# Optimization experiments

Measured on AMD Instinct MI355X. Metric: run time of the kernel, lower is better.

Reference implementation:

```python
import jax, jax.numpy as jnp
import numpy as np

D_MODEL = 1024
N_HEADS = 16
HEAD_DIM = D_MODEL // N_HEADS
D_FF = 4096
ROPE_RANK = 16
LN_EPS = 1e-5


def _ln(x, g, b):
    mu = jnp.mean(x, axis=-1, keepdims=True)
    var = jnp.mean((x - mu) ** 2, axis=-1, keepdims=True)
    return (x - mu) * jax.lax.rsqrt(var + LN_EPS) * g + b


def _rope(x, A, B_):
    # x: [B, T, D]; learned low-rank additive correction to sin/cos tables
    B, T, D = x.shape
    pos = jnp.arange(T, dtype=jnp.float32)
    theta = 1.0 / (10000.0 ** (jnp.arange(0, D, 2, dtype=jnp.float32) / D))  # [D/2]
    angles = pos[:, None] * theta[None, :]                                   # [T, D/2]
    sin_pos, cos_pos = jnp.sin(angles), jnp.cos(angles)
    base = jnp.concatenate([sin_pos, cos_pos], axis=-1)                      # [T, D]
    learned = (base @ A) @ B_                                                # [T, D]
    l_sin, l_cos = jnp.split(learned, 2, axis=-1)
    sin_f = sin_pos + l_sin                                                  # [T, D/2]
    cos_f = cos_pos + l_cos
    xe, xo = x[..., ::2], x[..., 1::2]
    re = xe * cos_f[None] - xo * sin_f[None]
    ro = xe * sin_f[None] + xo * cos_f[None]
    return jnp.stack([re, ro], axis=-1).reshape(B, T, D)


def setup_inputs() -> dict:
    key = jax.random.key(0)
    ks = jax.random.split(key, 20)
    B, T = 2, 2048
    s = 1.0 / np.sqrt(D_MODEL)
    sf = 1.0 / np.sqrt(D_FF)
    sr = 1.0 / np.sqrt(ROPE_RANK)
    return {
        "tgt": jax.random.normal(ks[0], (B, T, D_MODEL), jnp.float32),
        "Wq": jax.random.normal(ks[1], (D_MODEL, D_MODEL), jnp.float32) * s,
        "bq": jnp.zeros((D_MODEL,), jnp.float32),
        "Wk": jax.random.normal(ks[2], (D_MODEL, D_MODEL), jnp.float32) * s,
        "bk": jnp.zeros((D_MODEL,), jnp.float32),
        "Wv": jax.random.normal(ks[3], (D_MODEL, D_MODEL), jnp.float32) * s,
        "bv": jnp.zeros((D_MODEL,), jnp.float32),
        "Wo": jax.random.normal(ks[4], (D_MODEL, D_MODEL), jnp.float32) * s,
        "bo": jnp.zeros((D_MODEL,), jnp.float32),
        "W1": jax.random.normal(ks[5], (D_MODEL, D_FF), jnp.float32) * s,
        "b1": jnp.zeros((D_FF,), jnp.float32),
        "W2": jax.random.normal(ks[6], (D_FF, D_MODEL), jnp.float32) * sf,
        "b2": jnp.zeros((D_MODEL,), jnp.float32),
        "ln1_g": jnp.ones((D_MODEL,), jnp.float32),
        "ln1_b": jnp.zeros((D_MODEL,), jnp.float32),
        "ln2_g": jnp.ones((D_MODEL,), jnp.float32),
        "ln2_b": jnp.zeros((D_MODEL,), jnp.float32),
        "rope_A": jax.random.normal(ks[7], (D_MODEL, ROPE_RANK), jnp.float32) * s,
        "rope_B": jax.random.normal(ks[8], (ROPE_RANK, D_MODEL), jnp.float32) * sr,
    }


def reference(tgt, Wq, bq, Wk, bk, Wv, bv, Wo, bo, W1, b1, W2, b2,
              ln1_g, ln1_b, ln2_g, ln2_b, rope_A, rope_B):
    x = tgt
    B, T, D = x.shape
    q = _rope(x @ Wq + bq, rope_A, rope_B)
    k = _rope(x @ Wk + bk, rope_A, rope_B)
    v = x @ Wv + bv
    # [B, H, T, hd]
    q = q.reshape(B, T, N_HEADS, HEAD_DIM).transpose(0, 2, 1, 3)
    k = k.reshape(B, T, N_HEADS, HEAD_DIM).transpose(0, 2, 1, 3)
    v = v.reshape(B, T, N_HEADS, HEAD_DIM).transpose(0, 2, 1, 3)
    scores = jnp.einsum("bhqd,bhkd->bhqk", q, k) / np.sqrt(HEAD_DIM)
    attn = jax.nn.softmax(scores, axis=-1)  # no mask: module applies none
    ctx = jnp.einsum("bhqk,bhkd->bhqd", attn, v)
    ctx = ctx.transpose(0, 2, 1, 3).reshape(B, T, D)
    x = x + (ctx @ Wo + bo)
    x = _ln(x, ln1_g, ln1_b)
    ff = jax.nn.relu(x @ W1 + b1) @ W2 + b2
    x = _ln(x + ff, ln2_g, ln2_b)
    return x
```

## Files before the change

kernel.cpp:

```cpp
#include <hip/hip_runtime.h>
#include <math.h>

typedef unsigned short u16;
typedef unsigned int u32;
typedef __attribute__((ext_vector_type(8))) short short8v;
typedef __attribute__((ext_vector_type(4))) float f32x4;

__device__ __forceinline__ u16 f2bf(float f) {
    u32 u = __float_as_uint(f);
    u32 r = (u + 0x7fffu + ((u >> 16) & 1u)) >> 16;
    return (u16)r;
}

#define GLOAD_LDS(g, l)                                                        \
    __builtin_amdgcn_global_load_lds(                                          \
        (const __attribute__((address_space(1))) void*)(g),                    \
        (__attribute__((address_space(3))) void*)(l), 16, 0, 0)

#define SCHED_FENCE() __builtin_amdgcn_sched_barrier(0)

__global__ void cast_k(const float* __restrict__ x, u16* __restrict__ y) {
    const int gid = blockIdx.x * blockDim.x + threadIdx.x;
    float4 v = ((const float4*)x)[gid];
    ushort4 o;
    o.x = f2bf(v.x); o.y = f2bf(v.y); o.z = f2bf(v.z); o.w = f2bf(v.w);
    ((ushort4*)y)[gid] = o;
}

__global__ __launch_bounds__(256) void tcast_k(const float* __restrict__ S,
                                               u16* __restrict__ Dt,
                                               int K, int N) {
    __shared__ float tile[32][33];
    const int n0 = blockIdx.x * 32, k0 = blockIdx.y * 32;
    const int tx = threadIdx.x & 31, ty = threadIdx.x >> 5;
#pragma unroll
    for (int i = 0; i < 4; i++)
        tile[ty + 8 * i][tx] = S[(size_t)(k0 + ty + 8 * i) * N + n0 + tx];
    __syncthreads();
#pragma unroll
    for (int i = 0; i < 4; i++)
        Dt[(size_t)(n0 + ty + 8 * i) * K + k0 + tx] = f2bf(tile[tx][ty + 8 * i]);
}

__global__ __launch_bounds__(256) void vtrans_k(const u16* __restrict__ vv,
                                                u16* __restrict__ Vt) {
    __shared__ u16 tile[32][33];
    const int key0 = blockIdx.x * 32, d0 = blockIdx.y * 32, bh = blockIdx.z;
    const int b = bh >> 4, h = bh & 15;
    const int tx = threadIdx.x & 31, ty = threadIdx.x >> 5;
#pragma unroll
    for (int i = 0; i < 4; i++)
        tile[ty + 8 * i][tx] =
            vv[(size_t)(b * 2048 + key0 + ty + 8 * i) * 1024 + h * 64 + d0 + tx];
    __syncthreads();
#pragma unroll
    for (int i = 0; i < 4; i++) {
        const int d = d0 + ty + 8 * i;
        const int key = key0 + tx;
        const int ksw = (key & ~63) | ((((key >> 3) & 7) ^ (d & 7)) << 3) | (key & 7);
        Vt[((size_t)bh * 64 + d) * 2048 + ksw] = tile[tx][ty + 8 * i];
    }
}

#define ROPE_LOG2C (13.287712379549449f / 512.0f)

__global__ __launch_bounds__(256) void rope1_k(const float* __restrict__ A,
                                               float* __restrict__ P) {
    __shared__ float sc[16][17];
    __shared__ float cc[16][17];
    __shared__ float Als[16][17];
    __shared__ float Alc[16][17];
    const int tid = threadIdx.x;
    const int tt = tid >> 4, rr = tid & 15;
    const int t = blockIdx.x * 16 + tt;
    float acc = 0.f;
    for (int i0 = 0; i0 < 512; i0 += 16) {
        __syncthreads();
        {
            const int i = i0 + rr;
            const float th = exp2f(-(float)i * ROPE_LOG2C);
            const float ang = (float)t * th;
            sc[tt][rr] = sinf(ang);
            cc[tt][rr] = cosf(ang);
            Als[tt][rr] = A[(i0 + tt) * 16 + rr];
            Alc[tt][rr] = A[(512 + i0 + tt) * 16 + rr];
        }
        __syncthreads();
#pragma unroll
        for (int ii = 0; ii < 16; ++ii)
            acc = fmaf(sc[tt][ii], Als[ii][rr],
                       fmaf(cc[tt][ii], Alc[ii][rr], acc));
    }
    P[t * 16 + rr] = acc;
}

__global__ void rope2_k(const float* __restrict__ P, const float* __restrict__ Bw,
                        float* __restrict__ sf, float* __restrict__ cf) {
    const int gid = blockIdx.x * blockDim.x + threadIdx.x;
    if (gid >= 2048 * 512) return;
    const int t = gid >> 9, i = gid & 511;
    float ls = 0.f, lc = 0.f;
#pragma unroll
    for (int r = 0; r < 16; ++r) {
        const float p = P[t * 16 + r];
        ls = fmaf(p, Bw[r * 1024 + i], ls);
        lc = fmaf(p, Bw[r * 1024 + 512 + i], lc);
    }
    const float th = exp2f(-(float)i * ROPE_LOG2C);
    const float ang = (float)t * th;
    sf[gid] = sinf(ang) + ls;
    cf[gid] = cosf(ang) + lc;
}

__device__ __forceinline__ void xcd_tile(int L, int xn, int rn, int rm,
                                         int& tm, int& tn) {
    const int xcd = L & 7, i = L >> 3;
    const int cx = xcd % xn, cy = xcd / xn;
    tn = cx * rn + (i % rn);
    tm = cy * rm + (i / rn);
}

enum { EP_NONE = 0, EP_RELU = 3, EP_PART = 4 };

template <int EPI, bool CBF, int BN>
__global__ __launch_bounds__(256) void mgemm_k(
    const u16* __restrict__ A, const u16* __restrict__ Bt,
    const float* __restrict__ bias, void* __restrict__ Cp,
    void* __restrict__ Cp2, int M, int N, int K, int lda, int ldb,
    int xn, int rn, int rm, int mtiles) {
    constexpr int NT = BN / 32;
    __shared__ u16 As[3 * 128 * 32];
    __shared__ u16 Bs[3 * BN * 32];
    const int tid = threadIdx.x;
    const int w = tid >> 6, l = tid & 63;
    const int quad = l >> 4, lr = l & 15;
    const int wr = w >> 1, wc = w & 1;
    int tm, tn;
    xcd_tile(blockIdx.x, xn, rn, rm, tm, tn);
    int kh = 0;
    if (tm >= mtiles) { kh = 1; tm -= mtiles; }
    const u16* Ak = A + (size_t)kh * K;
    const u16* Bk = Bt + (size_t)kh * K;
    void* Co = kh ? Cp2 : Cp;
    const int m0 = tm * 128, n0 = tn * BN;

    const int srow = w * 16 + (l >> 2);
    const int scol = (((l & 3) ^ ((l >> 3) & 3)) * 8);
    const u16* ag0 = Ak + (size_t)(m0 + srow) * lda + scol;
    const u16* ag1 = Ak + (size_t)(m0 + 64 + srow) * lda + scol;
    const u16* bg0 = Bk + (size_t)(n0 + srow) * ldb + scol;
    const u16* bg1 = Bk + (size_t)(n0 + 64 + srow) * ldb + scol;

    f32x4 acc[4][NT];
#pragma unroll
    for (int i = 0; i < 4; i++)
#pragma unroll
        for (int j = 0; j < NT; j++) acc[i][j] = (f32x4)(0.0f);

    {
        GLOAD_LDS(ag0, As + w * 512);
        GLOAD_LDS(ag1, As + 2048 + w * 512);
        GLOAD_LDS(bg0, Bs + w * 512);
        if (BN == 128) GLOAD_LDS(bg1, Bs + 2048 + w * 512);
        GLOAD_LDS(ag0 + 32, As + 4096 + w * 512);
        GLOAD_LDS(ag1 + 32, As + 4096 + 2048 + w * 512);
        GLOAD_LDS(bg0 + 32, Bs + BN * 32 + w * 512);
        if (BN == 128) GLOAD_LDS(bg1 + 32, Bs + BN * 32 + 2048 + w * 512);
    }

    const int niter = K >> 5;
    const int xsw = ((lr >> 1) & 3) << 3;
    int bc = 0, bs = 2;
    for (int i = 0; i < niter; ++i) {
        SCHED_FENCE();
        if (i + 1 < niter) {
            if (BN == 128) asm volatile("s_waitcnt vmcnt(4) lgkmcnt(0)" ::: "memory");
            else           asm volatile("s_waitcnt vmcnt(3) lgkmcnt(0)" ::: "memory");
        } else {
            asm volatile("s_waitcnt vmcnt(0) lgkmcnt(0)" ::: "memory");
        }
        __builtin_amdgcn_s_barrier();
        SCHED_FENCE();
        if (i + 2 < niter) {
            const int kk = (i + 2) << 5;
            u16* Ab = As + bs * 4096;
            u16* Bb = Bs + bs * (BN * 32);
            GLOAD_LDS(ag0 + kk, Ab + w * 512);
            GLOAD_LDS(ag1 + kk, Ab + 2048 + w * 512);
            GLOAD_LDS(bg0 + kk, Bb + w * 512);
            if (BN == 128) GLOAD_LDS(bg1 + kk, Bb + 2048 + w * 512);
        }
        const u16* Ac = As + bc * 4096;
        const u16* Bc = Bs + bc * (BN * 32);
        short8v af[4], bf[NT];
#pragma unroll
        for (int mt = 0; mt < 4; ++mt)
            af[mt] = *(const short8v*)&Ac[(wr * 64 + mt * 16 + lr) * 32 +
                                          ((quad << 3) ^ xsw)];
#pragma unroll
        for (int nt = 0; nt < NT; ++nt)
            bf[nt] = *(const short8v*)&Bc[(wc * (BN / 2) + nt * 16 + lr) * 32 +
                                          ((quad << 3) ^ xsw)];
#pragma unroll
        for (int mt = 0; mt < 4; ++mt)
#pragma unroll
            for (int nt = 0; nt < NT; ++nt)
                acc[mt][nt] = __builtin_amdgcn_mfma_f32_16x16x32_bf16(
                    af[mt], bf[nt], acc[mt][nt], 0, 0, 0);
        bc = (bc == 2) ? 0 : bc + 1;
        bs = (bs == 2) ? 0 : bs + 1;
    }

#pragma unroll
    for (int mt = 0; mt < 4; ++mt) {
#pragma unroll
        for (int nt = 0; nt < NT; ++nt) {
            const int n = n0 + wc * (BN / 2) + nt * 16 + lr;
            const float bb = (EPI == EP_PART) ? 0.0f : bias[n];
#pragma unroll
            for (int reg = 0; reg < 4; ++reg) {
                const int m = m0 + wr * 64 + mt * 16 + quad * 4 + reg;
                float v = acc[mt][nt][reg] + bb;
                if (EPI == EP_RELU) v = fmaxf(v, 0.f);
                if (CBF) ((u16*)Co)[(size_t)m * N + n] = f2bf(v);
                else     ((float*)Co)[(size_t)m * N + n] = v;
            }
        }
    }
}

__global__ __launch_bounds__(256) void mqkv_k(
    const u16* __restrict__ A, const u16* __restrict__ Bt,
    const float* __restrict__ bq, const float* __restrict__ bk,
    const float* __restrict__ bv, const float* __restrict__ sf,
    const float* __restrict__ cf, u16* __restrict__ out) {
    const int K = 1024;
    __shared__ u16 As[3 * 128 * 32];
    __shared__ u16 Bs[3 * 128 * 32];
    const int tid = threadIdx.x;
    const int w = tid >> 6, l = tid & 63;
    const int quad = l >> 4, lr = l & 15;
    const int wr = w >> 1, wc = w & 1;
    int tm, tn;
    xcd_tile(blockIdx.x, 4, 6, 16, tm, tn);
    const int m0 = tm * 128, n0 = tn * 128;

    const int srow = w * 16 + (l >> 2);
    const int scol = (((l & 3) ^ ((l >> 3) & 3)) * 8);
    const u16* ag0 = A + (size_t)(m0 + srow) * K + scol;
    const u16* ag1 = A + (size_t)(m0 + 64 + srow) * K + scol;
    const u16* bg0 = Bt + (size_t)(n0 + srow) * K + scol;
    const u16* bg1 = Bt + (size_t)(n0 + 64 + srow) * K + scol;

    f32x4 acc[4][4];
#pragma unroll
    for (int i = 0; i < 4; i++)
#pragma unroll
        for (int j = 0; j < 4; j++) acc[i][j] = (f32x4)(0.0f);

    {
        GLOAD_LDS(ag0, As + w * 512);
        GLOAD_LDS(ag1, As + 2048 + w * 512);
        GLOAD_LDS(bg0, Bs + w * 512);
        GLOAD_LDS(bg1, Bs + 2048 + w * 512);
        GLOAD_LDS(ag0 + 32, As + 4096 + w * 512);
        GLOAD_LDS(ag1 + 32, As + 4096 + 2048 + w * 512);
        GLOAD_LDS(bg0 + 32, Bs + 4096 + w * 512);
        GLOAD_LDS(bg1 + 32, Bs + 4096 + 2048 + w * 512);
    }
    const int xsw = ((lr >> 1) & 3) << 3;
    int bc = 0, bsb = 2;
    for (int i = 0; i < 32; ++i) {
        SCHED_FENCE();
        if (i + 1 < 32) {
            asm volatile("s_waitcnt vmcnt(4) lgkmcnt(0)" ::: "memory");
        } else {
            asm volatile("s_waitcnt vmcnt(0) lgkmcnt(0)" ::: "memory");
        }
        __builtin_amdgcn_s_barrier();
        SCHED_FENCE();
        if (i + 2 < 32) {
            const int kk = (i + 2) << 5;
            u16* Ab = As + bsb * 4096;
            u16* Bb = Bs + bsb * 4096;
            GLOAD_LDS(ag0 + kk, Ab + w * 512);
            GLOAD_LDS(ag1 + kk, Ab + 2048 + w * 512);
            GLOAD_LDS(bg0 + kk, Bb + w * 512);
            GLOAD_LDS(bg1 + kk, Bb + 2048 + w * 512);
        }
        const u16* Ac = As + bc * 4096;
        const u16* Bc = Bs + bc * 4096;
        short8v af[4], bf[4];
#pragma unroll
        for (int mt = 0; mt < 4; ++mt)
            af[mt] = *(const short8v*)&Ac[(wr * 64 + mt * 16 + lr) * 32 +
                                          ((quad << 3) ^ xsw)];
#pragma unroll
        for (int nt = 0; nt < 4; ++nt)
            bf[nt] = *(const short8v*)&Bc[(wc * 64 + nt * 16 + lr) * 32 +
                                          ((quad << 3) ^ xsw)];
#pragma unroll
        for (int mt = 0; mt < 4; ++mt)
#pragma unroll
            for (int nt = 0; nt < 4; ++nt)
                acc[mt][nt] = __builtin_amdgcn_mfma_f32_16x16x32_bf16(
                    af[mt], bf[nt], acc[mt][nt], 0, 0, 0);
        bc = (bc == 2) ? 0 : bc + 1;
        bsb = (bsb == 2) ? 0 : bsb + 1;
    }

    const int which = n0 >> 10;
    const float* bias = which == 0 ? bq : (which == 1 ? bk : bv);
    const bool doRope = which < 2;
    u16* Cp = out + (size_t)which * 4096 * 1024;

#pragma unroll
    for (int mt = 0; mt < 4; ++mt) {
#pragma unroll
        for (int nt = 0; nt < 4; ++nt) {
            const int n = n0 + wc * 64 + nt * 16 + lr;
            const int col = n & 1023;
            const float bb = bias[col];
#pragma unroll
            for (int reg = 0; reg < 4; ++reg) {
                const int m = m0 + wr * 64 + mt * 16 + quad * 4 + reg;
                float v = acc[mt][nt][reg] + bb;
                const float partner = __shfl_xor(v, 1);
                int colw = col;
                if (doRope) {
                    const int t = m & 2047;
                    const int fi = col >> 1;
                    const float svv = sf[t * 512 + fi];
                    const float cvv = cf[t * 512 + fi];
                    v = (col & 1) ? fmaf(partner, svv, v * cvv)
                                  : fmaf(v, cvv, -partner * svv);
                    if (which == 0) v *= 0.125f;
                    colw = (col & ~63) | ((((col >> 3) & 7) ^ (m & 7)) << 3) |
                           (col & 7);
                }
                Cp[(size_t)m * 1024 + colw] = f2bf(v);
            }
        }
    }
}

__global__ __launch_bounds__(256, 3) void mattn_k(
    const u16* __restrict__ Q, const u16* __restrict__ Kg,
    const u16* __restrict__ Vt, u16* __restrict__ O) {
    __shared__ u16 QPs[128 * 64];
    __shared__ u16 Ks[2][64 * 64];
    __shared__ u16 Vs[2][64 * 64];
    const int tid = threadIdx.x;
    const int w = tid >> 6, l = tid & 63;
    const int quad = l >> 4, lr = l & 15;
    const int L = blockIdx.x;
    const int bh = (L & 7) * 4 + ((L >> 3) & 3);
    const int b = bh >> 4, h = bh & 15;
    const int row0 = (L >> 5) * 128;
    const size_t base = (size_t)b * 2048 * 1024 + (size_t)h * 64;
    const size_t vbase = (size_t)bh * 64 * 2048;

    const int dr = l >> 3;
    const int dc = (l & 7) * 8;
    const int g0 = w * 2, g1 = g0 + 1;
    const u16* kg0 = Kg + base + (size_t)(g0 * 8 + dr) * 1024 + dc;
    const u16* kg1 = Kg + base + (size_t)(g1 * 8 + dr) * 1024 + dc;
    const u16* vg0 = Vt + vbase + (size_t)(g0 * 8 + dr) * 2048 + dc;
    const u16* vg1 = Vt + vbase + (size_t)(g1 * 8 + dr) * 2048 + dc;

#pragma unroll
    for (int j = 0; j < 4; ++j) {
        const int g = w * 4 + j;
        GLOAD_LDS(Q + base + (size_t)(row0 + g * 8 + dr) * 1024 + dc,
                  QPs + g * 512);
    }
    GLOAD_LDS(kg0, Ks[0] + g0 * 512);
    GLOAD_LDS(kg1, Ks[0] + g1 * 512);
    GLOAD_LDS(vg0, Vs[0] + g0 * 512);
    GLOAD_LDS(vg1, Vs[0] + g1 * 512);
    __syncthreads();

    const int rsw = lr & 7;
    short8v qf[2][2];
#pragma unroll
    for (int ntq = 0; ntq < 2; ++ntq) {
        const int qr = w * 32 + ntq * 16 + lr;
#pragma unroll
        for (int kh = 0; kh < 2; ++kh)
            qf[ntq][kh] = *(const short8v*)&QPs[qr * 64 +
                (((kh * 4 + quad) ^ rsw) << 3)];
    }

    f32x4 o_acc[2][4];
#pragma unroll
    for (int i = 0; i < 2; ++i)
#pragma unroll
        for (int j = 0; j < 4; ++j) o_acc[i][j] = (f32x4)(0.0f);
    float lsum[2] = {0.f, 0.f};

    for (int i = 0; i < 32; ++i) {
        __syncthreads();
        if (i + 1 < 32) {
            const size_t kro = (size_t)((i + 1) << 6) * 1024;
            const int kco = (i + 1) << 6;
            u16* Kb = Ks[(i + 1) & 1];
            u16* Vb = Vs[(i + 1) & 1];
            GLOAD_LDS(kg0 + kro, Kb + g0 * 512);
            GLOAD_LDS(kg1 + kro, Kb + g1 * 512);
            GLOAD_LDS(vg0 + kco, Vb + g0 * 512);
            GLOAD_LDS(vg1 + kco, Vb + g1 * 512);
        }
        const u16* Kc = Ks[i & 1];
        const u16* Vc = Vs[i & 1];

        f32x4 s[4][2];
#pragma unroll
        for (int mt = 0; mt < 4; ++mt)
#pragma unroll
            for (int ntq = 0; ntq < 2; ++ntq) s[mt][ntq] = (f32x4)(0.0f);
#pragma unroll
        for (int mt = 0; mt < 4; ++mt) {
            const int kr = mt * 16 + lr;
            const short8v kf0 = *(const short8v*)&Kc[kr * 64 + ((quad ^ rsw) << 3)];
            const short8v kf1 = *(const short8v*)&Kc[kr * 64 + (((quad + 4) ^ rsw) << 3)];
#pragma unroll
            for (int ntq = 0; ntq < 2; ++ntq) {
                s[mt][ntq] = __builtin_amdgcn_mfma_f32_16x16x32_bf16(
                    kf0, qf[ntq][0], s[mt][ntq], 0, 0, 0);
                s[mt][ntq] = __builtin_amdgcn_mfma_f32_16x16x32_bf16(
                    kf1, qf[ntq][1], s[mt][ntq], 0, 0, 0);
            }
        }

#pragma unroll
        for (int ntq = 0; ntq < 2; ++ntq) {
            const int prow = w * 32 + ntq * 16 + lr;
#pragma unroll
            for (int mt = 0; mt < 4; ++mt) {
                const float e0 = __expf(s[mt][ntq][0]);
                const float e1 = __expf(s[mt][ntq][1]);
                const float e2 = __expf(s[mt][ntq][2]);
                const float e3 = __expf(s[mt][ntq][3]);
                lsum[ntq] += (e0 + e1) + (e2 + e3);
                u32 p01, p23;
                asm("v_cvt_pk_bf16_f32 %0, %1, %2" : "=v"(p01) : "v"(e0), "v"(e1));
                asm("v_cvt_pk_bf16_f32 %0, %1, %2" : "=v"(p23) : "v"(e2), "v"(e3));
                uint2 pv; pv.x = p01; pv.y = p23;
                *(uint2*)&QPs[prow * 64 +
                              (((mt * 2 + (quad >> 1)) ^ rsw) << 3) +
                              (quad & 1) * 4] = pv;
            }
        }

        short8v vf[4][2];
#pragma unroll
        for (int ntd = 0; ntd < 4; ++ntd) {
            const int vr = ntd * 16 + lr;
            vf[ntd][0] = *(const short8v*)&Vc[vr * 64 + ((quad ^ rsw) << 3)];
            vf[ntd][1] = *(const short8v*)&Vc[vr * 64 + (((quad + 4) ^ rsw) << 3)];
        }
        short8v pf[2][2];
#pragma unroll
        for (int mtq = 0; mtq < 2; ++mtq) {
            const int prow = w * 32 + mtq * 16 + lr;
            pf[mtq][0] = *(const short8v*)&QPs[prow * 64 + ((quad ^ rsw) << 3)];
            pf[mtq][1] = *(const short8v*)&QPs[prow * 64 + (((quad + 4) ^ rsw) << 3)];
        }
#pragma unroll
        for (int mtq = 0; mtq < 2; ++mtq)
#pragma unroll
            for (int ntd = 0; ntd < 4; ++ntd) {
                o_acc[mtq][ntd] = __builtin_amdgcn_mfma_f32_16x16x32_bf16(
                    pf[mtq][0], vf[ntd][0], o_acc[mtq][ntd], 0, 0, 0);
                o_acc[mtq][ntd] = __builtin_amdgcn_mfma_f32_16x16x32_bf16(
                    pf[mtq][1], vf[ntd][1], o_acc[mtq][ntd], 0, 0, 0);
            }
    }

    float rden[2];
#pragma unroll
    for (int ntq = 0; ntq < 2; ++ntq) {
        float t = lsum[ntq];
        t += __shfl_xor(t, 16);
        t += __shfl_xor(t, 32);
        rden[ntq] = 1.0f / t;
    }
#pragma unroll
    for (int mtq = 0; mtq < 2; ++mtq) {
#pragma unroll
        for (int reg = 0; reg < 4; ++reg) {
            const float dsc = __shfl(rden[mtq], quad * 4 + reg);
            const int m = row0 + w * 32 + mtq * 16 + quad * 4 + reg;
#pragma unroll
            for (int ntd = 0; ntd < 4; ++ntd)
                O[base + (size_t)m * 1024 + ntd * 16 + lr] =
                    f2bf(o_acc[mtq][ntd][reg] * dsc);
        }
    }
}

__global__ __launch_bounds__(256) void lnf_k(
    const float* __restrict__ X, const float* __restrict__ P0,
    const float* __restrict__ P1, const float* __restrict__ cb,
    const float* __restrict__ g, const float* __restrict__ bb,
    float* __restrict__ outf, u16* __restrict__ outb) {
    const int row = blockIdx.x, tid = threadIdx.x;
    const size_t off = (size_t)row * 1024 + tid * 4;
    float4 xv = *(const float4*)&X[off];
    float4 p0 = *(const float4*)&P0[off];
    float4 p1 = *(const float4*)&P1[off];
    float4 c4 = *(const float4*)&cb[tid * 4];
    xv.x += p0.x + p1.x + c4.x;
    xv.y += p0.y + p1.y + c4.y;
    xv.z += p0.z + p1.z + c4.z;
    xv.w += p0.w + p1.w + c4.w;
    float s = xv.x + xv.y + xv.z + xv.w;
    float s2 = xv.x * xv.x + xv.y * xv.y + xv.z * xv.z + xv.w * xv.w;
#pragma unroll
    for (int msk = 32; msk >= 1; msk >>= 1) {
        s += __shfl_xor(s, msk);
        s2 += __shfl_xor(s2, msk);
    }
    __shared__ float red[8];
    const int wv = tid >> 6;
    if ((tid & 63) == 0) { red[wv] = s; red[wv + 4] = s2; }
    __syncthreads();
    s = red[0] + red[1] + red[2] + red[3];
    s2 = red[4] + red[5] + red[6] + red[7];
    const float mu = s * (1.f / 1024.f);
    float var = s2 * (1.f / 1024.f) - mu * mu;
    var = fmaxf(var, 0.f);
    const float rstd = rsqrtf(var + 1e-5f);
    float4 g4 = *(const float4*)&g[tid * 4];
    float4 b4 = *(const float4*)&bb[tid * 4];
    float o0 = (xv.x - mu) * rstd * g4.x + b4.x;
    float o1 = (xv.y - mu) * rstd * g4.y + b4.y;
    float o2 = (xv.z - mu) * rstd * g4.z + b4.z;
    float o3 = (xv.w - mu) * rstd * g4.w + b4.w;
    if (outf)
        *(float4*)(outf + off) = make_float4(o0, o1, o2, o3);
    if (outb) {
        ushort4 ov;
        ov.x = f2bf(o0); ov.y = f2bf(o1); ov.z = f2bf(o2); ov.w = f2bf(o3);
        *(ushort4*)(outb + off) = ov;
    }
}

extern "C" void kernel_launch(void* const* d_in, const int* in_sizes, int n_in,
                              void* d_out, int out_size, void* d_ws, size_t ws_size,
                              hipStream_t stream) {
    const float* tgt = (const float*)d_in[0];
    const float* Wq  = (const float*)d_in[1];
    const float* bq  = (const float*)d_in[2];
    const float* Wk  = (const float*)d_in[3];
    const float* bk  = (const float*)d_in[4];
    const float* Wv  = (const float*)d_in[5];
    const float* bv  = (const float*)d_in[6];
    const float* Wo  = (const float*)d_in[7];
    const float* bo  = (const float*)d_in[8];
    const float* W1  = (const float*)d_in[9];
    const float* b1  = (const float*)d_in[10];
    const float* W2  = (const float*)d_in[11];
    const float* b2  = (const float*)d_in[12];
    const float* g1  = (const float*)d_in[13];
    const float* be1 = (const float*)d_in[14];
    const float* g2  = (const float*)d_in[15];
    const float* be2 = (const float*)d_in[16];
    const float* rA  = (const float*)d_in[17];
    const float* rB  = (const float*)d_in[18];

    const int M = 4096, D = 1024, DFF = 4096;
    const size_t MD = (size_t)M * D;
    const size_t MB = 1u << 20;
    char* wsb = (char*)d_ws;

    u16* q    = (u16*)wsb;
    u16* vv   = q + 2 * MD;
    u16* ctx  = (u16*)(wsb + 16 * MB);
    u16* Vt   = (u16*)(wsb + 24 * MB);
    u16* h    = q;
    float* PW0 = (float*)wsb;
    float* PW1 = (float*)(wsb + 32 * MB);
    float* PF0 = (float*)(wsb + 64 * MB);
    float* PF1 = (float*)(wsb + 32 * MB);
    float* sfp = (float*)(wsb + 32 * MB);
    float* cfp = sfp + (size_t)2048 * 512;
    u16* tgtb = (u16*)(wsb + 40 * MB);
    float* x1  = (float*)(wsb + 48 * MB);
    u16* x1b  = (u16*)(wsb + 64 * MB);
    u16* Wqt  = (u16*)(wsb + 64 * MB);
    u16* Wkt  = (u16*)(wsb + 66 * MB);
    u16* Wvt  = (u16*)(wsb + 68 * MB);
    u16* Wot  = (u16*)(wsb + 70 * MB);
    u16* W1t  = (u16*)(wsb + 72 * MB);
    u16* W2t  = (u16*)(wsb + 80 * MB);
    float* Pp = (float*)wsb;

    cast_k<<<dim3(4096), dim3(256), 0, stream>>>(tgt, tgtb);
    tcast_k<<<dim3(32, 32),  dim3(256), 0, stream>>>(Wq, Wqt, D, D);
    tcast_k<<<dim3(32, 32),  dim3(256), 0, stream>>>(Wk, Wkt, D, D);
    tcast_k<<<dim3(32, 32),  dim3(256), 0, stream>>>(Wv, Wvt, D, D);
    tcast_k<<<dim3(32, 32),  dim3(256), 0, stream>>>(Wo, Wot, D, D);
    tcast_k<<<dim3(128, 32), dim3(256), 0, stream>>>(W1, W1t, D, DFF);
    tcast_k<<<dim3(32, 128), dim3(256), 0, stream>>>(W2, W2t, DFF, D);
    rope1_k<<<dim3(128), dim3(256), 0, stream>>>(rA, Pp);
    rope2_k<<<dim3(4096), dim3(256), 0, stream>>>(Pp, rB, sfp, cfp);

    mqkv_k<<<dim3(768), dim3(256), 0, stream>>>(
        tgtb, Wqt, bq, bk, bv, sfp, cfp, q);

    vtrans_k<<<dim3(64, 2, 32), dim3(256), 0, stream>>>(vv, Vt);

    mattn_k<<<dim3(512), dim3(256), 0, stream>>>(q, q + MD, Vt, ctx);

    mgemm_k<EP_PART, false, 128><<<dim3(512), dim3(256), 0, stream>>>(
        ctx, Wot, nullptr, PW0, PW1, M, D, 512, D, D, 1, 8, 8, 32);
    lnf_k<<<dim3(4096), dim3(256), 0, stream>>>(
        tgt, PW0, PW1, bo, g1, be1, x1, x1b);
    mgemm_k<EP_RELU, true, 128><<<dim3(1024), dim3(256), 0, stream>>>(
        x1b, W1t, b1, h, nullptr, M, DFF, D, D, D, 4, 8, 16, 1 << 20);
    mgemm_k<EP_PART, false, 128><<<dim3(512), dim3(256), 0, stream>>>(
        h, W2t, nullptr, PF0, PF1, M, D, 2048, DFF, DFF, 1, 8, 8, 32);
    lnf_k<<<dim3(4096), dim3(256), 0, stream>>>(
        x1, PF0, PF1, b2, g2, be2, (float*)d_out, nullptr);

    (void)in_sizes; (void)n_in; (void)out_size; (void)ws_size;
}
```

Baseline: 428.4 us.

## Use 256x256 tiles with 8-wave blocks for QKV and FFN1 GEMMs

Replaces the 128x128, 4-wave QKV GEMM and the generic FFN1 GEMM with new 512-thread kernels that each compute a 256x256 output tile. They use a double-buffered LDS pipeline with split LDS fragment loads, MFMA work interleaved between two barriers, and s_setprio raised around the second MFMA half. The larger tile raises arithmetic intensity and cuts global/L2 traffic per FLOP. In exchange it uses more registers per thread (32 accumulators), launches far fewer blocks (192 and 256 on a 256-CU part), and drops from triple to double buffering.

```diff
diff --git a/kernel.cpp b/kernel.cpp
--- a/kernel.cpp
+++ b/kernel.cpp
@@ -229,85 +229,117 @@
     }
 }
 
-__global__ __launch_bounds__(256) void mqkv_k(
+#define G256_PROLOGUE()                                                        \
+    const int tid = threadIdx.x;                                               \
+    const int w = tid >> 6, l = tid & 63;                                      \
+    const int quad = l >> 4, lr = l & 15;                                      \
+    const int wr = w >> 2, wc = w & 3;                                         \
+    const int srow = w * 16 + (l >> 2);                                        \
+    const int scol = (((l & 3) ^ ((l >> 3) & 3)) * 8);                         \
+    const int xsw = ((lr >> 1) & 3) << 3;
+
+#define G256_STAGE(Ab, Bb, kt)                                                 \
+    do {                                                                       \
+        GLOAD_LDS(bg0 + ((kt) << 5), (Bb) + w * 512);                          \
+        GLOAD_LDS(bg1 + ((kt) << 5), (Bb) + 4096 + w * 512);                   \
+        GLOAD_LDS(ag0 + ((kt) << 5), (Ab) + w * 512);                          \
+        GLOAD_LDS(ag1 + ((kt) << 5), (Ab) + 4096 + w * 512);                   \
+    } while (0)
+
+#define G256_LOOP(K)                                                           \
+    f32x4 acc[8][4];                                                           \
+    _Pragma("unroll") for (int i = 0; i < 8; i++)                              \
+        _Pragma("unroll") for (int j = 0; j < 4; j++) acc[i][j] = (f32x4)(0.0f);\
+    G256_STAGE(As[0], Bs[0], 0);                                               \
+    G256_STAGE(As[1], Bs[1], 1);                                               \
+    const int nt_ = (K) >> 5;                                                  \
+    for (int t = 0; t < nt_; ++t) {                                            \
+        SCHED_FENCE();                                                         \
+        if (t + 1 < nt_) asm volatile("s_waitcnt vmcnt(4)" ::: "memory");      \
+        else             asm volatile("s_waitcnt vmcnt(0)" ::: "memory");      \
+        __builtin_amdgcn_s_barrier();                                          \
+        SCHED_FENCE();                                                         \
+        const u16* Ac = As[t & 1];                                             \
+        const u16* Bc = Bs[t & 1];                                             \
+        short8v af[8], bf[4];                                                  \
+        _Pragma("unroll") for (int nn = 0; nn < 4; ++nn)                       \
+            bf[nn] = *(const short8v*)&Bc[(wc * 64 + nn * 16 + lr) * 32 +      \
+                                          ((quad << 3) ^ xsw)];                \
+        _Pragma("unroll") for (int mm = 0; mm < 4; ++mm)                       \
+            af[mm] = *(const short8v*)&Ac[(wr * 128 + mm * 16 + lr) * 32 +     \
+                                          ((quad << 3) ^ xsw)];                \
+        SCHED_FENCE();                                                         \
+        _Pragma("unroll") for (int mm = 4; mm < 8; ++mm)                       \
+            af[mm] = *(const short8v*)&Ac[(wr * 128 + mm * 16 + lr) * 32 +     \
+                                          ((quad << 3) ^ xsw)];                \
+        SCHED_FENCE();                                                         \
+        asm volatile("s_waitcnt lgkmcnt(4)" ::: "memory");                     \
+        SCHED_FENCE();                                                         \
+        _Pragma("unroll") for (int mm = 0; mm < 4; ++mm)                       \
+            _Pragma("unroll") for (int nn = 0; nn < 4; ++nn)                   \
+                acc[mm][nn] = __builtin_amdgcn_mfma_f32_16x16x32_bf16(         \
+                    af[mm], bf[nn], acc[mm][nn], 0, 0, 0);                     \
+        SCHED_FENCE();                                                         \
+        asm volatile("s_waitcnt lgkmcnt(0)" ::: "memory");                     \
+        SCHED_FENCE();                                                         \
+        __builtin_amdgcn_s_barrier();                                          \
+        SCHED_FENCE();                                                         \
+        if (t + 2 < nt_) { G256_STAGE(As[t & 1], Bs[t & 1], t + 2); }          \
+        SCHED_FENCE();                                                         \
+        __builtin_amdgcn_s_setprio(1);                                         \
+        _Pragma("unroll") for (int mm = 4; mm < 8; ++mm)                       \
+            _Pragma("unroll") for (int nn = 0; nn < 4; ++nn)                   \
+                acc[mm][nn] = __builtin_amdgcn_mfma_f32_16x16x32_bf16(         \
+                    af[mm], bf[nn], acc[mm][nn], 0, 0, 0);                     \
+        __builtin_amdgcn_s_setprio(0);                                         \
+    }
+
+__global__ __launch_bounds__(512, 2) void gffn1_k(
+    const u16* __restrict__ A, const u16* __restrict__ Bt,
+    const float* __restrict__ bias, u16* __restrict__ Cp) {
+    __shared__ u16 As[2][256 * 32];
+    __shared__ u16 Bs[2][256 * 32];
+    G256_PROLOGUE();
+    int tm, tn;
+    xcd_tile(blockIdx.x, 4, 4, 8, tm, tn);
+    const int m0 = tm * 256, n0 = tn * 256;
+    const u16* ag0 = A + (size_t)(m0 + srow) * 1024 + scol;
+    const u16* ag1 = A + (size_t)(m0 + 128 + srow) * 1024 + scol;
+    const u16* bg0 = Bt + (size_t)(n0 + srow) * 1024 + scol;
+    const u16* bg1 = Bt + (size_t)(n0 + 128 + srow) * 1024 + scol;
+    G256_LOOP(1024);
+#pragma unroll
+    for (int mm = 0; mm < 8; ++mm) {
+#pragma unroll
+        for (int nn = 0; nn < 4; ++nn) {
+            const int n = n0 + wc * 64 + nn * 16 + lr;
+            const float bb = bias[n];
+#pragma unroll
+            for (int reg = 0; reg < 4; ++reg) {
+                const int m = m0 + wr * 128 + mm * 16 + quad * 4 + reg;
+                const float v = fmaxf(acc[mm][nn][reg] + bb, 0.f);
+                Cp[(size_t)m * 4096 + n] = f2bf(v);
+            }
+        }
+    }
+}
+
+__global__ __launch_bounds__(512, 2) void gqkv_k(
     const u16* __restrict__ A, const u16* __restrict__ Bt,
     const float* __restrict__ bq, const float* __restrict__ bk,
     const float* __restrict__ bv, const float* __restrict__ sf,
     const float* __restrict__ cf, u16* __restrict__ out) {
-    const int K = 1024;
-    __shared__ u16 As[3 * 128 * 32];
-    __shared__ u16 Bs[3 * 128 * 32];
-    const int tid = threadIdx.x;
-    const int w = tid >> 6, l = tid & 63;
-    const int quad = l >> 4, lr = l & 15;
-    const int wr = w >> 1, wc = w & 1;
+    __shared__ u16 As[2][256 * 32];
+    __shared__ u16 Bs[2][256 * 32];
+    G256_PROLOGUE();
     int tm, tn;
-    xcd_tile(blockIdx.x, 4, 6, 16, tm, tn);
-    const int m0 = tm * 128, n0 = tn * 128;
-
-    const int srow = w * 16 + (l >> 2);
-    const int scol = (((l & 3) ^ ((l >> 3) & 3)) * 8);
-    const u16* ag0 = A + (size_t)(m0 + srow) * K + scol;
-    const u16* ag1 = A + (size_t)(m0 + 64 + srow) * K + scol;
-    const u16* bg0 = Bt + (size_t)(n0 + srow) * K + scol;
-    const u16* bg1 = Bt + (size_t)(n0 + 64 + srow) * K + scol;
-
-    f32x4 acc[4][4];
-#pragma unroll
-    for (int i = 0; i < 4; i++)
-#pragma unroll
-        for (int j = 0; j < 4; j++) acc[i][j] = (f32x4)(0.0f);
-
-    {
-        GLOAD_LDS(ag0, As + w * 512);
-        GLOAD_LDS(ag1, As + 2048 + w * 512);
-        GLOAD_LDS(bg0, Bs + w * 512);
-        GLOAD_LDS(bg1, Bs + 2048 + w * 512);
-        GLOAD_LDS(ag0 + 32, As + 4096 + w * 512);
-        GLOAD_LDS(ag1 + 32, As + 4096 + 2048 + w * 512);
-        GLOAD_LDS(bg0 + 32, Bs + 4096 + w * 512);
-        GLOAD_LDS(bg1 + 32, Bs + 4096 + 2048 + w * 512);
-    }
-    const int xsw = ((lr >> 1) & 3) << 3;
-    int bc = 0, bsb = 2;
-    for (int i = 0; i < 32; ++i) {
-        SCHED_FENCE();
-        if (i + 1 < 32) {
-            asm volatile("s_waitcnt vmcnt(4) lgkmcnt(0)" ::: "memory");
-        } else {
-            asm volatile("s_waitcnt vmcnt(0) lgkmcnt(0)" ::: "memory");
-        }
-        __builtin_amdgcn_s_barrier();
-        SCHED_FENCE();
-        if (i + 2 < 32) {
-            const int kk = (i + 2) << 5;
-            u16* Ab = As + bsb * 4096;
-            u16* Bb = Bs + bsb * 4096;
-            GLOAD_LDS(ag0 + kk, Ab + w * 512);
-            GLOAD_LDS(ag1 + kk, Ab + 2048 + w * 512);
-            GLOAD_LDS(bg0 + kk, Bb + w * 512);
-            GLOAD_LDS(bg1 + kk, Bb + 2048 + w * 512);
-        }
-        const u16* Ac = As + bc * 4096;
-        const u16* Bc = Bs + bc * 4096;
-        short8v af[4], bf[4];
-#pragma unroll
-        for (int mt = 0; mt < 4; ++mt)
-            af[mt] = *(const short8v*)&Ac[(wr * 64 + mt * 16 + lr) * 32 +
-                                          ((quad << 3) ^ xsw)];
-#pragma unroll
-        for (int nt = 0; nt < 4; ++nt)
-            bf[nt] = *(const short8v*)&Bc[(wc * 64 + nt * 16 + lr) * 32 +
-                                          ((quad << 3) ^ xsw)];
-#pragma unroll
-        for (int mt = 0; mt < 4; ++mt)
-#pragma unroll
-            for (int nt = 0; nt < 4; ++nt)
-                acc[mt][nt] = __builtin_amdgcn_mfma_f32_16x16x32_bf16(
-                    af[mt], bf[nt], acc[mt][nt], 0, 0, 0);
-        bc = (bc == 2) ? 0 : bc + 1;
-        bsb = (bsb == 2) ? 0 : bsb + 1;
-    }
+    xcd_tile(blockIdx.x, 4, 3, 8, tm, tn);
+    const int m0 = tm * 256, n0 = tn * 256;
+    const u16* ag0 = A + (size_t)(m0 + srow) * 1024 + scol;
+    const u16* ag1 = A + (size_t)(m0 + 128 + srow) * 1024 + scol;
+    const u16* bg0 = Bt + (size_t)(n0 + srow) * 1024 + scol;
+    const u16* bg1 = Bt + (size_t)(n0 + 128 + srow) * 1024 + scol;
+    G256_LOOP(1024);
 
     const int which = n0 >> 10;
     const float* bias = which == 0 ? bq : (which == 1 ? bk : bv);
@@ -315,16 +347,16 @@
     u16* Cp = out + (size_t)which * 4096 * 1024;
 
 #pragma unroll
-    for (int mt = 0; mt < 4; ++mt) {
-#pragma unroll
-        for (int nt = 0; nt < 4; ++nt) {
-            const int n = n0 + wc * 64 + nt * 16 + lr;
+    for (int mm = 0; mm < 8; ++mm) {
+#pragma unroll
+        for (int nn = 0; nn < 4; ++nn) {
+            const int n = n0 + wc * 64 + nn * 16 + lr;
             const int col = n & 1023;
             const float bb = bias[col];
 #pragma unroll
             for (int reg = 0; reg < 4; ++reg) {
-                const int m = m0 + wr * 64 + mt * 16 + quad * 4 + reg;
-                float v = acc[mt][nt][reg] + bb;
+                const int m = m0 + wr * 128 + mm * 16 + quad * 4 + reg;
+                float v = acc[mm][nn][reg] + bb;
                 const float partner = __shfl_xor(v, 1);
                 int colw = col;
                 if (doRope) {
@@ -606,7 +638,7 @@
     rope1_k<<<dim3(128), dim3(256), 0, stream>>>(rA, Pp);
     rope2_k<<<dim3(4096), dim3(256), 0, stream>>>(Pp, rB, sfp, cfp);
 
-    mqkv_k<<<dim3(768), dim3(256), 0, stream>>>(
+    gqkv_k<<<dim3(192), dim3(512), 0, stream>>>(
         tgtb, Wqt, bq, bk, bv, sfp, cfp, q);
 
     vtrans_k<<<dim3(64, 2, 32), dim3(256), 0, stream>>>(vv, Vt);
@@ -617,8 +649,7 @@
         ctx, Wot, nullptr, PW0, PW1, M, D, 512, D, D, 1, 8, 8, 32);
     lnf_k<<<dim3(4096), dim3(256), 0, stream>>>(
         tgt, PW0, PW1, bo, g1, be1, x1, x1b);
-    mgemm_k<EP_RELU, true, 128><<<dim3(1024), dim3(256), 0, stream>>>(
-        x1b, W1t, b1, h, nullptr, M, DFF, D, D, D, 4, 8, 16, 1 << 20);
+    gffn1_k<<<dim3(256), dim3(512), 0, stream>>>(x1b, W1t, b1, h);
     mgemm_k<EP_PART, false, 128><<<dim3(512), dim3(256), 0, stream>>>(
         h, W2t, nullptr, PF0, PF1, M, D, 2048, DFF, DFF, 1, 8, 8, 32);
     lnf_k<<<dim3(4096), dim3(256), 0, stream>>>(
```

After: 448.8 us. 1.05x slower.
